# Performance work log

Hardware: AMD Instinct MI355X
Metric: run time of the kernel (lower is better)

Reference implementation:

```python
import jax, jax.numpy as jnp
import numpy as np

N_NODES = 100000
N_EDGES = 1200000
HIDDEN = 64


def gcn_conv(x, edge_index, W, b):
    """PyG-style GCNConv: add self-loops, symmetric norm, aggregate, linear."""
    n = x.shape[0]
    h = x @ W  # [N, out]
    src = jnp.concatenate([edge_index[0], jnp.arange(n)])  # self-loops
    dst = jnp.concatenate([edge_index[1], jnp.arange(n)])
    ones = jnp.ones(src.shape[0], dtype=x.dtype)
    deg = jax.ops.segment_sum(ones, dst, num_segments=n)  # in-degree incl. self-loop
    dinv = jnp.where(deg > 0, jax.lax.rsqrt(deg), 0.0)
    norm = dinv[src] * dinv[dst]  # [E+N]
    msgs = h[src] * norm[:, None]  # gather + scale, [E+N, out]
    out = jax.ops.segment_sum(msgs, dst, num_segments=n)  # scatter-add
    return out + b


def setup_inputs() -> dict:
    key = jax.random.key(0)
    k1, k2, k3, k4 = jax.random.split(key, 4)
    x = jax.random.normal(k1, (N_NODES, 1), dtype=jnp.float32)
    edge_index = jax.random.randint(k2, (2, N_EDGES), 0, N_NODES, dtype=jnp.int64)
    glorot1 = (6.0 / (1 + HIDDEN)) ** 0.5
    glorot2 = (6.0 / (HIDDEN + 1)) ** 0.5
    W1 = jax.random.uniform(k3, (1, HIDDEN), jnp.float32, -glorot1, glorot1)
    b1 = jnp.zeros((HIDDEN,), jnp.float32)
    W2 = jax.random.uniform(k4, (HIDDEN, 1), jnp.float32, -glorot2, glorot2)
    b2 = jnp.zeros((1,), jnp.float32)
    return {"x": x, "edge_index": edge_index, "W1": W1, "b1": b1, "W2": W2, "b2": b2}


def reference(x, edge_index, W1, b1, W2, b2):
    h = gcn_conv(x, edge_index, W1, b1)
    h = jax.nn.relu(h)
    # F.dropout(training=self.training): eval mode -> identity
    out = gcn_conv(h, edge_index, W2, b2)
    return out
```

## Files before the change

### kernel.cpp

```cpp
#include <hip/hip_runtime.h>

#define HIDDEN 64
#define LOGB 9
#define BSN 512
#define NTILES 256
#define NTS 1024
#define NTE 1024
#define MAXBK 256
#define CAPT 64
#define SRCBITS 17
#define SENT 0xFFFFFFFFu
#define GL 8
#define SGRP (NTS / GL)

__global__ __launch_bounds__(NTS) void k_sort(const int* __restrict__ src,
                                              const int* __restrict__ dst,
                                              int e, int nbuck,
                                              unsigned* __restrict__ sw) {
    __shared__ int lcnt[MAXBK];
    __shared__ unsigned cells[MAXBK * CAPT];
    const int t = blockIdx.x, tid = threadIdx.x;
    for (int g = tid; g < nbuck; g += NTS) lcnt[g] = 0;
    __syncthreads();
    const int Q = e >> 2;
    const int qlo = (int)((long long)Q * t / NTILES);
    const int qhi = (int)((long long)Q * (t + 1) / NTILES);
    for (int q = qlo + tid; q < qhi; q += NTS) {
        int4 s4 = ((const int4*)src)[q];
        int4 d4 = ((const int4*)dst)[q];
        { int d = d4.x, g = d >> LOGB; int p = atomicAdd(&lcnt[g], 1);
          if (p < CAPT) cells[g * CAPT + p] =
              ((unsigned)(d & (BSN - 1)) << SRCBITS) | (unsigned)s4.x; }
        { int d = d4.y, g = d >> LOGB; int p = atomicAdd(&lcnt[g], 1);
          if (p < CAPT) cells[g * CAPT + p] =
              ((unsigned)(d & (BSN - 1)) << SRCBITS) | (unsigned)s4.y; }
        { int d = d4.z, g = d >> LOGB; int p = atomicAdd(&lcnt[g], 1);
          if (p < CAPT) cells[g * CAPT + p] =
              ((unsigned)(d & (BSN - 1)) << SRCBITS) | (unsigned)s4.z; }
        { int d = d4.w, g = d >> LOGB; int p = atomicAdd(&lcnt[g], 1);
          if (p < CAPT) cells[g * CAPT + p] =
              ((unsigned)(d & (BSN - 1)) << SRCBITS) | (unsigned)s4.w; }
    }
    if (t == 0) {
        for (int i = (Q << 2) + tid; i < e; i += NTS) {
            int d = dst[i], g = d >> LOGB;
            int p = atomicAdd(&lcnt[g], 1);
            if (p < CAPT) cells[g * CAPT + p] =
                ((unsigned)(d & (BSN - 1)) << SRCBITS) | (unsigned)src[i];
        }
    }
    __syncthreads();
    const int grp = tid >> 3, lg = tid & (GL - 1);
    for (int g = grp; g < nbuck; g += SGRP) {
        int cnt = lcnt[g]; if (cnt > CAPT) cnt = CAPT;
        for (int p = cnt + lg; p < CAPT; p += GL) cells[g * CAPT + p] = SENT;
        const uint4* lc = (const uint4*)&cells[g * CAPT];
        uint4* gseg = (uint4*)(sw + ((size_t)g * NTILES + t) * CAPT);
#pragma unroll
        for (int q = lg; q < (CAPT >> 2); q += GL) gseg[q] = lc[q];
    }
}

__global__ __launch_bounds__(NTE) void k_deg_prep(const unsigned* __restrict__ sw,
                                                  const float* __restrict__ x,
                                                  float* __restrict__ dinv,
                                                  float* __restrict__ xs,
                                                  int n) {
    __shared__ float lacc[BSN];
    const int g = blockIdx.x, tid = threadIdx.x;
    if (tid < BSN) lacc[tid] = 0.0f;
    __syncthreads();
    const uint4* row = (const uint4*)(sw + (size_t)g * NTILES * CAPT);
    const int nq = NTILES * CAPT / 4;
    for (int q = tid; q < nq; q += NTE) {
        uint4 w4 = row[q];
        unsigned l0 = w4.x >> SRCBITS; if (l0 < BSN) atomicAdd(&lacc[l0], 1.0f);
        unsigned l1 = w4.y >> SRCBITS; if (l1 < BSN) atomicAdd(&lacc[l1], 1.0f);
        unsigned l2 = w4.z >> SRCBITS; if (l2 < BSN) atomicAdd(&lacc[l2], 1.0f);
        unsigned l3 = w4.w >> SRCBITS; if (l3 < BSN) atomicAdd(&lacc[l3], 1.0f);
    }
    __syncthreads();
    const int node = (g << LOGB) + tid;
    if (tid < BSN && node < n) {
        float d = rsqrtf(1.0f + lacc[tid]);
        dinv[node] = d;
        xs[node] = x[node] * d;
    }
}

__global__ __launch_bounds__(NTE) void k_scat_mlp(const unsigned* __restrict__ sw,
    const float* __restrict__ dinv, const float* __restrict__ xs,
    const float* __restrict__ W1, const float* __restrict__ b1,
    const float* __restrict__ W2, float* __restrict__ h2s, int n) {
    __shared__ float lacc[BSN];
    __shared__ float swt[3 * HIDDEN];
    const int g = blockIdx.x, tid = threadIdx.x;
    if (tid < BSN) lacc[tid] = 0.0f;
    if (tid >= BSN && tid < BSN + 3 * HIDDEN) {
        int j = tid - BSN;
        swt[j] = (j < HIDDEN) ? W1[j]
               : (j < 2 * HIDDEN) ? b1[j - HIDDEN] : W2[j - 2 * HIDDEN];
    }
    __syncthreads();
    const unsigned SM = (1u << SRCBITS) - 1;
    const uint4* row = (const uint4*)(sw + (size_t)g * NTILES * CAPT);
    const int nq = NTILES * CAPT / 4;
    for (int q = tid; q < nq; q += NTE) {
        uint4 w4 = row[q];
        unsigned l0 = w4.x >> SRCBITS; if (l0 < BSN) atomicAdd(&lacc[l0], xs[w4.x & SM]);
        unsigned l1 = w4.y >> SRCBITS; if (l1 < BSN) atomicAdd(&lacc[l1], xs[w4.y & SM]);
        unsigned l2 = w4.z >> SRCBITS; if (l2 < BSN) atomicAdd(&lacc[l2], xs[w4.z & SM]);
        unsigned l3 = w4.w >> SRCBITS; if (l3 < BSN) atomicAdd(&lacc[l3], xs[w4.w & SM]);
    }
    __syncthreads();
    const int node = (g << LOGB) + tid;
    if (tid < BSN && node < n) {
        float di = dinv[node];
        float s1 = di * (lacc[tid] + xs[node]);
        float h = 0.0f;
#pragma unroll
        for (int j = 0; j < HIDDEN; ++j)
            h += fmaxf(fmaf(s1, swt[j], swt[HIDDEN + j]), 0.0f) * swt[2 * HIDDEN + j];
        h2s[node] = h * di;
    }
}

__global__ __launch_bounds__(NTE) void k_scat_out(const unsigned* __restrict__ sw,
    const float* __restrict__ dinv, const float* __restrict__ h2s,
    const float* __restrict__ b2, float* __restrict__ out, int n) {
    __shared__ float lacc[BSN];
    const int g = blockIdx.x, tid = threadIdx.x;
    if (tid < BSN) lacc[tid] = 0.0f;
    __syncthreads();
    const unsigned SM = (1u << SRCBITS) - 1;
    const uint4* row = (const uint4*)(sw + (size_t)g * NTILES * CAPT);
    const int nq = NTILES * CAPT / 4;
    for (int q = tid; q < nq; q += NTE) {
        uint4 w4 = row[q];
        unsigned l0 = w4.x >> SRCBITS; if (l0 < BSN) atomicAdd(&lacc[l0], h2s[w4.x & SM]);
        unsigned l1 = w4.y >> SRCBITS; if (l1 < BSN) atomicAdd(&lacc[l1], h2s[w4.y & SM]);
        unsigned l2 = w4.z >> SRCBITS; if (l2 < BSN) atomicAdd(&lacc[l2], h2s[w4.z & SM]);
        unsigned l3 = w4.w >> SRCBITS; if (l3 < BSN) atomicAdd(&lacc[l3], h2s[w4.w & SM]);
    }
    __syncthreads();
    const int node = (g << LOGB) + tid;
    if (tid < BSN && node < n)
        out[node] = dinv[node] * (lacc[tid] + h2s[node]) + b2[0];
}

__global__ void f_init(float* deg, float* agg, int n) {
    int i = blockIdx.x * blockDim.x + threadIdx.x;
    if (i < n) { deg[i] = 1.0f; agg[i] = 0.0f; }
}
__global__ void f_deg(const int* __restrict__ dst, float* deg, int e) {
    int i = blockIdx.x * blockDim.x + threadIdx.x;
    if (i < e) atomicAdd(&deg[dst[i]], 1.0f);
}
__global__ void f_prep(const float* __restrict__ x, float* deg,
                       float* __restrict__ xs, int n) {
    int i = blockIdx.x * blockDim.x + threadIdx.x;
    if (i < n) { float d = rsqrtf(deg[i]); deg[i] = d; xs[i] = x[i] * d; }
}
__global__ void f_scat(const int* __restrict__ src, const int* __restrict__ dst,
                       const float* __restrict__ vals, float* agg, int e) {
    int i = blockIdx.x * blockDim.x + threadIdx.x;
    if (i < e) atomicAdd(&agg[dst[i]], vals[src[i]]);
}
__global__ void f_mlp(const float* __restrict__ dinv, const float* __restrict__ xs,
                      float* agg, const float* __restrict__ W1,
                      const float* __restrict__ b1, const float* __restrict__ W2,
                      float* __restrict__ h2s, int n) {
    __shared__ float sW1[HIDDEN], sb1[HIDDEN], sW2[HIDDEN];
    if (threadIdx.x < HIDDEN) {
        sW1[threadIdx.x] = W1[threadIdx.x];
        sb1[threadIdx.x] = b1[threadIdx.x];
        sW2[threadIdx.x] = W2[threadIdx.x];
    }
    __syncthreads();
    int i = blockIdx.x * blockDim.x + threadIdx.x;
    if (i >= n) return;
    float di = dinv[i];
    float s1 = di * (agg[i] + xs[i]);
    agg[i] = 0.0f;
    float h = 0.0f;
#pragma unroll
    for (int j = 0; j < HIDDEN; ++j)
        h += fmaxf(fmaf(s1, sW1[j], sb1[j]), 0.0f) * sW2[j];
    h2s[i] = h * di;
}
__global__ void f_out(const float* __restrict__ dinv, const float* __restrict__ h2s,
                      const float* __restrict__ agg, const float* __restrict__ b2,
                      float* __restrict__ out, int n) {
    int i = blockIdx.x * blockDim.x + threadIdx.x;
    if (i < n) out[i] = dinv[i] * (agg[i] + h2s[i]) + b2[0];
}

extern "C" void kernel_launch(void* const* d_in, const int* in_sizes, int n_in,
                              void* d_out, int out_size, void* d_ws, size_t ws_size,
                              hipStream_t stream) {
    const float* x  = (const float*)d_in[0];
    const int*   ei = (const int*)d_in[1];
    const float* W1 = (const float*)d_in[2];
    const float* b1 = (const float*)d_in[3];
    const float* W2 = (const float*)d_in[4];
    const float* b2 = (const float*)d_in[5];
    float* out = (float*)d_out;

    const int n = in_sizes[0];
    const int e = in_sizes[1] / 2;
    const int* src = ei;
    const int* dst = ei + e;

    const int nbuck = (n + BSN - 1) >> LOGB;
    const size_t need = ((size_t)3 * n + (size_t)nbuck * NTILES * CAPT)
                        * sizeof(int);
    const bool cap_ok = (long long)e * 2 <= (long long)NTILES * nbuck * CAPT;

    if (nbuck >= 1 && nbuck <= MAXBK && n <= (1 << SRCBITS) &&
        e >= 4 && cap_ok && ws_size >= need) {
        float* dinv  = (float*)d_ws;
        float* xs    = dinv + n;
        float* h2s   = xs + n;
        unsigned* sw = (unsigned*)(h2s + n);

        k_sort    <<<NTILES, NTS, 0, stream>>>(src, dst, e, nbuck, sw);
        k_deg_prep<<<nbuck,  NTE, 0, stream>>>(sw, x, dinv, xs, n);
        k_scat_mlp<<<nbuck,  NTE, 0, stream>>>(sw, dinv, xs, W1, b1, W2, h2s, n);
        k_scat_out<<<nbuck,  NTE, 0, stream>>>(sw, dinv, h2s, b2, out, n);
    } else {
        const int BT = 256;
        const int gn = (n + BT - 1) / BT;
        const int ge = (e + BT - 1) / BT;
        float* dinv = (float*)d_ws;
        float* xs   = dinv + n;
        float* h2s  = xs + n;
        float* agg  = h2s + n;
        f_init<<<gn, BT, 0, stream>>>(dinv, agg, n);
        f_deg <<<ge, BT, 0, stream>>>(dst, dinv, e);
        f_prep<<<gn, BT, 0, stream>>>(x, dinv, xs, n);
        f_scat<<<ge, BT, 0, stream>>>(src, dst, xs, agg, e);
        f_mlp <<<gn, BT, 0, stream>>>(dinv, xs, agg, W1, b1, W2, h2s, n);
        f_scat<<<ge, BT, 0, stream>>>(src, dst, h2s, agg, e);
        f_out <<<gn, BT, 0, stream>>>(dinv, h2s, agg, b2, out, n);
    }
}
```

Measured before the change: 45.94 us.

## Compact per-bucket edge rows with global atomic cursors instead of padded tile slots

The sort kernel now appends each tile's bucket slice, padded only to a multiple of four, into a compact per-bucket row. Placement uses a global atomic cursor, replacing a fixed slot per tile and bucket that was mostly sentinel padding. The three scatter kernels read only the filled part of each row, which cuts the global memory they stream. Tiles are halved to 128 with larger per-tile cell capacity, and a memset of the cursors adds a launch. The sort kernel now uses only 128 workgroups, and the larger cell array raises its LDS footprint.

Measured after the change: 52.96 us. +15.3%, slower.

```diff
diff --git a/kernel.cpp b/kernel.cpp
--- a/kernel.cpp
+++ b/kernel.cpp
@@ -3,11 +3,12 @@
 #define HIDDEN 64
 #define LOGB 9
 #define BSN 512
-#define NTILES 256
+#define NTILES 128
 #define NTS 1024
 #define NTE 1024
-#define MAXBK 256
-#define CAPT 64
+#define MAXBK 200
+#define CAPT 96
+#define ROWCAP 12288
 #define SRCBITS 17
 #define SENT 0xFFFFFFFFu
 #define GL 8
@@ -16,7 +17,8 @@
 __global__ __launch_bounds__(NTS) void k_sort(const int* __restrict__ src,
                                               const int* __restrict__ dst,
                                               int e, int nbuck,
-                                              unsigned* __restrict__ sw) {
+                                              unsigned* __restrict__ sw,
+                                              int* __restrict__ gcur) {
     __shared__ int lcnt[MAXBK];
     __shared__ unsigned cells[MAXBK * CAPT];
     const int t = blockIdx.x, tid = threadIdx.x;
@@ -53,15 +55,21 @@
     const int grp = tid >> 3, lg = tid & (GL - 1);
     for (int g = grp; g < nbuck; g += SGRP) {
         int cnt = lcnt[g]; if (cnt > CAPT) cnt = CAPT;
-        for (int p = cnt + lg; p < CAPT; p += GL) cells[g * CAPT + p] = SENT;
-        const uint4* lc = (const uint4*)&cells[g * CAPT];
-        uint4* gseg = (uint4*)(sw + ((size_t)g * NTILES + t) * CAPT);
-#pragma unroll
-        for (int q = lg; q < (CAPT >> 2); q += GL) gseg[q] = lc[q];
+        const int cp = (cnt + 3) & ~3;
+        for (int p = cnt + lg; p < cp; p += GL) cells[g * CAPT + p] = SENT;
+        int pos = 0;
+        if (lg == 0 && cp > 0) pos = atomicAdd(&gcur[g], cp);
+        pos = __shfl(pos, 0, GL);
+        if (cp > 0 && pos + cp <= ROWCAP) {
+            const uint4* lc = (const uint4*)&cells[g * CAPT];
+            uint4* gseg = (uint4*)(sw + (size_t)g * ROWCAP + pos);
+            for (int q = lg; q < (cp >> 2); q += GL) gseg[q] = lc[q];
+        }
     }
 }
 
 __global__ __launch_bounds__(NTE) void k_deg_prep(const unsigned* __restrict__ sw,
+                                                  const int* __restrict__ gcur,
                                                   const float* __restrict__ x,
                                                   float* __restrict__ dinv,
                                                   float* __restrict__ xs,
@@ -70,9 +78,9 @@
     const int g = blockIdx.x, tid = threadIdx.x;
     if (tid < BSN) lacc[tid] = 0.0f;
     __syncthreads();
-    const uint4* row = (const uint4*)(sw + (size_t)g * NTILES * CAPT);
-    const int nq = NTILES * CAPT / 4;
-    for (int q = tid; q < nq; q += NTE) {
+    int tot = gcur[g]; if (tot > ROWCAP) tot = ROWCAP;
+    const uint4* row = (const uint4*)(sw + (size_t)g * ROWCAP);
+    for (int q = tid; q < (tot >> 2); q += NTE) {
         uint4 w4 = row[q];
         unsigned l0 = w4.x >> SRCBITS; if (l0 < BSN) atomicAdd(&lacc[l0], 1.0f);
         unsigned l1 = w4.y >> SRCBITS; if (l1 < BSN) atomicAdd(&lacc[l1], 1.0f);
@@ -89,9 +97,10 @@
 }
 
 __global__ __launch_bounds__(NTE) void k_scat_mlp(const unsigned* __restrict__ sw,
-    const float* __restrict__ dinv, const float* __restrict__ xs,
-    const float* __restrict__ W1, const float* __restrict__ b1,
-    const float* __restrict__ W2, float* __restrict__ h2s, int n) {
+    const int* __restrict__ gcur, const float* __restrict__ dinv,
+    const float* __restrict__ xs, const float* __restrict__ W1,
+    const float* __restrict__ b1, const float* __restrict__ W2,
+    float* __restrict__ h2s, int n) {
     __shared__ float lacc[BSN];
     __shared__ float swt[3 * HIDDEN];
     const int g = blockIdx.x, tid = threadIdx.x;
@@ -103,9 +112,9 @@
     }
     __syncthreads();
     const unsigned SM = (1u << SRCBITS) - 1;
-    const uint4* row = (const uint4*)(sw + (size_t)g * NTILES * CAPT);
-    const int nq = NTILES * CAPT / 4;
-    for (int q = tid; q < nq; q += NTE) {
+    int tot = gcur[g]; if (tot > ROWCAP) tot = ROWCAP;
+    const uint4* row = (const uint4*)(sw + (size_t)g * ROWCAP);
+    for (int q = tid; q < (tot >> 2); q += NTE) {
         uint4 w4 = row[q];
         unsigned l0 = w4.x >> SRCBITS; if (l0 < BSN) atomicAdd(&lacc[l0], xs[w4.x & SM]);
         unsigned l1 = w4.y >> SRCBITS; if (l1 < BSN) atomicAdd(&lacc[l1], xs[w4.y & SM]);
@@ -126,16 +135,17 @@
 }
 
 __global__ __launch_bounds__(NTE) void k_scat_out(const unsigned* __restrict__ sw,
-    const float* __restrict__ dinv, const float* __restrict__ h2s,
-    const float* __restrict__ b2, float* __restrict__ out, int n) {
+    const int* __restrict__ gcur, const float* __restrict__ dinv,
+    const float* __restrict__ h2s, const float* __restrict__ b2,
+    float* __restrict__ out, int n) {
     __shared__ float lacc[BSN];
     const int g = blockIdx.x, tid = threadIdx.x;
     if (tid < BSN) lacc[tid] = 0.0f;
     __syncthreads();
     const unsigned SM = (1u << SRCBITS) - 1;
-    const uint4* row = (const uint4*)(sw + (size_t)g * NTILES * CAPT);
-    const int nq = NTILES * CAPT / 4;
-    for (int q = tid; q < nq; q += NTE) {
+    int tot = gcur[g]; if (tot > ROWCAP) tot = ROWCAP;
+    const uint4* row = (const uint4*)(sw + (size_t)g * ROWCAP);
+    for (int q = tid; q < (tot >> 2); q += NTE) {
         uint4 w4 = row[q];
         unsigned l0 = w4.x >> SRCBITS; if (l0 < BSN) atomicAdd(&lacc[l0], h2s[w4.x & SM]);
         unsigned l1 = w4.y >> SRCBITS; if (l1 < BSN) atomicAdd(&lacc[l1], h2s[w4.y & SM]);
@@ -212,21 +222,26 @@
     const int* dst = ei + e;
 
     const int nbuck = (n + BSN - 1) >> LOGB;
-    const size_t need = ((size_t)3 * n + (size_t)nbuck * NTILES * CAPT)
+    const size_t need = ((size_t)3 * n + (size_t)nbuck * ROWCAP + nbuck)
                         * sizeof(int);
-    const bool cap_ok = (long long)e * 2 <= (long long)NTILES * nbuck * CAPT;
+    const bool cell_ok = (long long)e * 2 <= (long long)NTILES * nbuck * CAPT;
+    const bool row_ok = ((long long)e / nbuck + 4LL * NTILES) * 3 / 2 <= ROWCAP;
 
     if (nbuck >= 1 && nbuck <= MAXBK && n <= (1 << SRCBITS) &&
-        e >= 4 && cap_ok && ws_size >= need) {
+        e >= 4 && cell_ok && row_ok && ws_size >= need) {
         float* dinv  = (float*)d_ws;
         float* xs    = dinv + n;
         float* h2s   = xs + n;
         unsigned* sw = (unsigned*)(h2s + n);
-
-        k_sort    <<<NTILES, NTS, 0, stream>>>(src, dst, e, nbuck, sw);
-        k_deg_prep<<<nbuck,  NTE, 0, stream>>>(sw, x, dinv, xs, n);
-        k_scat_mlp<<<nbuck,  NTE, 0, stream>>>(sw, dinv, xs, W1, b1, W2, h2s, n);
-        k_scat_out<<<nbuck,  NTE, 0, stream>>>(sw, dinv, h2s, b2, out, n);
+        int* gcur    = (int*)(sw + (size_t)nbuck * ROWCAP);
+
+        hipMemsetAsync(gcur, 0, (size_t)nbuck * sizeof(int), stream);
+        k_sort    <<<NTILES, NTS, 0, stream>>>(src, dst, e, nbuck, sw, gcur);
+        k_deg_prep<<<nbuck,  NTE, 0, stream>>>(sw, gcur, x, dinv, xs, n);
+        k_scat_mlp<<<nbuck,  NTE, 0, stream>>>(sw, gcur, dinv, xs,
+                                               W1, b1, W2, h2s, n);
+        k_scat_out<<<nbuck,  NTE, 0, stream>>>(sw, gcur, dinv, h2s,
+                                               b2, out, n);
     } else {
         const int BT = 256;
         const int gn = (n + BT - 1) / BT;
```
